# Performance work log

Measured on AMD Instinct MI355X. Metric: run time of the kernel, lower is better.

## Reference

```python
import jax, jax.numpy as jnp
import numpy as np

NUM_FREQS = 6

def posenc(x, num_freqs):
    freqs = (2.0 ** jnp.arange(num_freqs)).astype(x.dtype)  # [F]
    ang = x[..., None] * freqs                               # [N, D, F]
    enc = jnp.concatenate([jnp.sin(ang), jnp.cos(ang)], axis=-1)  # [N, D, 2F]
    return enc.reshape(x.shape[0], -1)

def setup_inputs() -> dict:
    key = jax.random.key(0)
    k1, k2, k3 = jax.random.split(key, 3)
    N, D, C = 200000, 6, 256
    E = D * 2 * NUM_FREQS  # 72
    X = jax.random.normal(k1, (N, D), dtype=jnp.float32)
    linear_mappings = jax.random.normal(k2, (3 * C, E), dtype=jnp.float32) * 0.05
    centroids = jax.random.normal(k3, (C, 3), dtype=jnp.float32)
    return {"X": X, "linear_mappings": linear_mappings, "centroids": centroids}

def reference(X, linear_mappings, centroids):
    N = X.shape[0]
    encoded_X = posenc(X, NUM_FREQS)                         # [N, E]
    rgb_clusters = encoded_X @ linear_mappings.T             # [N, 3C]
    rgb_clusters = rgb_clusters.reshape(N, -1, 3)            # [N, C, 3]
    # scores = centroids @ X[:, :3].T  -> softmax over clusters per point
    scores = X[:, :3] @ centroids.T                          # [N, C] (== scores.T in torch code)
    attention_weights = jax.nn.softmax(scores, axis=-1)      # [N, C]
    # torch does diagonal(attn @ rgb_clusters).T == per-row contraction:
    rgb = jnp.einsum('nc,ncd->nd', attention_weights, rgb_clusters)  # [N, 3]
    return rgb
```

## Files before the change

### kernel.cpp

```cpp
#include <hip/hip_runtime.h>
#include <math.h>


#define NCLUST   256
#define M_BLK    128
#define THREADS  256
#define NTILES   15
#define BG_BYTES (NTILES * 8 * 64 * 16)
#define ENC_STRIDE 168

typedef __attribute__((ext_vector_type(8))) short bfrag_t;
typedef __attribute__((ext_vector_type(4))) float cfrag_t;

static __device__ __forceinline__ unsigned int f2bf_u(float f) {
    unsigned int u = __float_as_uint(f);
    u += 0x7fffu + ((u >> 16) & 1u);
    return u >> 16;
}
static __device__ __forceinline__ unsigned int f2bf2(float lo, float hi) {
    return f2bf_u(lo) | (f2bf_u(hi) << 16);
}
static __device__ __forceinline__ float bf2f(unsigned short s) {
    return __uint_as_float(((unsigned int)s) << 16);
}
static __device__ __forceinline__ void glds16(const void* g, void* l) {
    __builtin_amdgcn_global_load_lds(
        (const __attribute__((address_space(1))) unsigned int*)g,
        (__attribute__((address_space(3))) unsigned int*)l, 16, 0, 0);
}

__global__ void prep_kernel(const float* __restrict__ W, uint4* __restrict__ Bg) {
    const int u = blockIdx.x * 256 + threadIdx.x;
    if (u >= NTILES * 8 * 64) return;
    const int lane = u & 63, ks = (u >> 6) & 7, tile = u >> 9;
    const int ln = lane & 15, q = lane >> 4;
    const int jp = tile * 16 + ln;
    const int d  = jp / 80;
    const int e  = jp - d * 80;
    const int c0 = ks * 32 + q * 8;
    unsigned int w[4] = {0u, 0u, 0u, 0u};
    if (e < 72) {
#pragma unroll
        for (int i = 0; i < 4; ++i) {
            float f0 = W[((c0 + 2 * i)     * 3 + d) * 72 + e];
            float f1 = W[((c0 + 2 * i + 1) * 3 + d) * 72 + e];
            w[i] = f2bf2(f0, f1);
        }
    }
    Bg[u] = make_uint4(w[0], w[1], w[2], w[3]);
}

__global__ __launch_bounds__(THREADS, 2) void rgb_attn_mfma(
    const float* __restrict__ X,
    const float* __restrict__ cent,
    const void* __restrict__ Bg,
    float* __restrict__ out, int N)
{
    __shared__ __align__(16) unsigned char encL[M_BLK * ENC_STRIDE];
    __shared__ __align__(16) unsigned char ABbuf[16384];
    __shared__ float denomL[M_BLK * 2];

    const int tid  = threadIdx.x;
    const int lane = tid & 63;
    const int wv   = tid >> 6;
    const int q    = lane >> 4;
    const int ln   = lane & 15;

    const int pt  = tid & 127;
    const int h   = tid >> 7;
    const int gpt = blockIdx.x * M_BLK + pt;
    const int gp  = (gpt < N) ? gpt : (N - 1);

    float x[6];
#pragma unroll
    for (int k = 0; k < 6; ++k) x[k] = X[gp * 6 + k];

    {
        const int row = tid >> 1, half = tid & 1;
        *(uint2*)(encL + row * ENC_STRIDE + 144 + half * 8) = make_uint2(0u, 0u);
    }
#pragma unroll
    for (int k = 0; k < 3; ++k) {
        const int dd = 3 * h + k;
        const float xv = x[dd];
        float s0,c0,s1,c1,s2,c2,s3,c3,s4,c4,s5,c5;
        __sincosf(xv *  1.0f, &s0, &c0);
        __sincosf(xv *  2.0f, &s1, &c1);
        __sincosf(xv *  4.0f, &s2, &c2);
        __sincosf(xv *  8.0f, &s3, &c3);
        __sincosf(xv * 16.0f, &s4, &c4);
        __sincosf(xv * 32.0f, &s5, &c5);
        unsigned char* rp = encL + pt * ENC_STRIDE + dd * 24;
        *(uint2*)(rp +  0) = make_uint2(f2bf2(s0, s1), f2bf2(s2, s3));
        *(uint2*)(rp +  8) = make_uint2(f2bf2(s4, s5), f2bf2(c0, c1));
        *(uint2*)(rp + 16) = make_uint2(f2bf2(c2, c3), f2bf2(c4, c5));
    }

    bfrag_t afrag[2][8];
    float dpart = 0.0f;
    uint4* AB4 = (uint4*)ABbuf;
#pragma unroll
    for (int p = 0; p < 4; ++p) {
        unsigned int pk[16];
#pragma unroll
        for (int i = 0; i < 16; ++i) {
            const int c0 = p * 64 + h * 32 + 2 * i;
            float sa = fmaf(x[0], cent[c0*3+0], fmaf(x[1], cent[c0*3+1], x[2]*cent[c0*3+2]));
            float sb = fmaf(x[0], cent[c0*3+3], fmaf(x[1], cent[c0*3+4], x[2]*cent[c0*3+5]));
            float ea = __expf(sa), eb_ = __expf(sb);
            dpart += ea + eb_;
            pk[i] = f2bf2(ea, eb_);
        }
        const int bu = ((pt >> 4) * 2 + h) * 64 + (pt & 15);
#pragma unroll
        for (int qq = 0; qq < 4; ++qq)
            AB4[bu + qq * 16] = make_uint4(pk[qq*4+0], pk[qq*4+1], pk[qq*4+2], pk[qq*4+3]);
        if (p == 3) denomL[pt * 2 + h] = dpart;
        __syncthreads();
#pragma unroll
        for (int mt = 0; mt < 2; ++mt)
#pragma unroll
            for (int kw = 0; kw < 2; ++kw)
                afrag[mt][2*p+kw] = *(const bfrag_t*)
                    (ABbuf + (((2*wv+mt)*2 + kw)*64 + lane)*16);
        __syncthreads();
    }

    float part[3][2][4] = {};

#define CONSUME_TILE(T, CT) { \
        cfrag_t a0 = {0.f,0.f,0.f,0.f}, a1 = {0.f,0.f,0.f,0.f}; \
        _Pragma("unroll") \
        for (int ks = 0; ks < 8; ++ks) { \
            const bfrag_t b = *(const bfrag_t*) \
                (ABbuf + (((CT)*8 + ks)*64 + lane)*16); \
            a0 = __builtin_amdgcn_mfma_f32_16x16x32_bf16(afrag[0][ks], b, a0, 0,0,0); \
            a1 = __builtin_amdgcn_mfma_f32_16x16x32_bf16(afrag[1][ks], b, a1, 0,0,0); \
        } \
        const int ebx = ((T) % 5) * 16 + ln; \
        _Pragma("unroll") \
        for (int mt = 0; mt < 2; ++mt) \
        _Pragma("unroll") \
        for (int r = 0; r < 4; ++r) { \
            const int pm = (2*wv + mt)*16 + q*4 + r; \
            const unsigned short us = *(const unsigned short*)(encL + pm*ENC_STRIDE + ebx*2); \
            part[(T)/5][mt][r] = fmaf((mt ? a1[r] : a0[r]), bf2f(us), part[(T)/5][mt][r]); \
        } \
    }

#define STAGE_CHUNK(CC, UNITS) { \
        __syncthreads(); \
        _Pragma("unroll") \
        for (int i = 0; i < 256; i += 64) { \
            if (i < (UNITS) / 4) { \
                const int u = wv * ((UNITS) / 4) + i + lane; \
                glds16((const char*)Bg + ((CC)*1024 + u)*16, (char*)ABbuf + u*16); \
            } } \
        __syncthreads(); \
    }

#define DO_CHUNK_FULL(CC) { \
        STAGE_CHUNK(CC, 1024); \
        CONSUME_TILE(2*(CC), 0); \
        CONSUME_TILE(2*(CC)+1, 1); \
    }

    DO_CHUNK_FULL(0) DO_CHUNK_FULL(1) DO_CHUNK_FULL(2) DO_CHUNK_FULL(3)
    DO_CHUNK_FULL(4) DO_CHUNK_FULL(5) DO_CHUNK_FULL(6)
    { STAGE_CHUNK(7, 512); CONSUME_TILE(14, 0); }

#pragma unroll
    for (int mask = 1; mask <= 8; mask <<= 1)
#pragma unroll
        for (int d = 0; d < 3; ++d)
#pragma unroll
            for (int mt = 0; mt < 2; ++mt)
#pragma unroll
                for (int r = 0; r < 4; ++r)
                    part[d][mt][r] += __shfl_xor(part[d][mt][r], mask, 64);

    if (ln == 0) {
#pragma unroll
        for (int mt = 0; mt < 2; ++mt)
#pragma unroll
            for (int r = 0; r < 4; ++r) {
                const int pm = (2*wv + mt)*16 + q*4 + r;
                const int g  = blockIdx.x * M_BLK + pm;
                if (g < N) {
                    const float inv = 1.0f / (denomL[pm*2] + denomL[pm*2+1]);
                    out[g*3+0] = part[0][mt][r] * inv;
                    out[g*3+1] = part[1][mt][r] * inv;
                    out[g*3+2] = part[2][mt][r] * inv;
                }
            }
    }
}

__global__ __launch_bounds__(256) void rgb_attn_fallback(
    const float* __restrict__ X, const float* __restrict__ W,
    const float* __restrict__ cent, float* __restrict__ out, int N)
{
    const int n = blockIdx.x * 256 + threadIdx.x;
    const bool valid = (n < N);
    float x[6];
#pragma unroll
    for (int k = 0; k < 6; ++k) x[k] = valid ? X[n * 6 + k] : 0.0f;
    float enc[72];
#pragma unroll
    for (int d = 0; d < 6; ++d)
#pragma unroll
        for (int f = 0; f < 6; ++f) {
            float s, c;
            __sincosf(x[d] * (float)(1 << f), &s, &c);
            enc[d*12+f] = s; enc[d*12+6+f] = c;
        }
    float acc0 = 0, acc1 = 0, acc2 = 0, denom = 0;
#pragma unroll 1
    for (int c = 0; c < NCLUST; ++c) {
        float s = fmaf(x[0], cent[c*3], fmaf(x[1], cent[c*3+1], x[2]*cent[c*3+2]));
        float ew = __expf(s);
        const float* w = W + c * 216;
        float d0 = 0, d1 = 0, d2 = 0;
#pragma unroll
        for (int e = 0; e < 72; ++e) {
            float ee = enc[e];
            d0 = fmaf(ee, w[e], d0);
            d1 = fmaf(ee, w[72 + e], d1);
            d2 = fmaf(ee, w[144 + e], d2);
        }
        denom += ew;
        acc0 = fmaf(ew, d0, acc0); acc1 = fmaf(ew, d1, acc1); acc2 = fmaf(ew, d2, acc2);
    }
    if (valid) {
        float inv = 1.0f / denom;
        out[n*3+0] = acc0*inv; out[n*3+1] = acc1*inv; out[n*3+2] = acc2*inv;
    }
}

extern "C" void kernel_launch(void* const* d_in, const int* in_sizes, int n_in,
                              void* d_out, int out_size, void* d_ws, size_t ws_size,
                              hipStream_t stream)
{
    const float* X    = (const float*)d_in[0];
    const float* W    = (const float*)d_in[1];
    const float* cent = (const float*)d_in[2];
    float* out = (float*)d_out;
    const int N = in_sizes[0] / 6;

    if (ws_size >= (size_t)BG_BYTES) {
        uint4* Bg = (uint4*)d_ws;
        prep_kernel<<<(NTILES * 8 * 64 + 255) / 256, 256, 0, stream>>>(W, Bg);
        const int blocks = (N + M_BLK - 1) / M_BLK;
        rgb_attn_mfma<<<blocks, THREADS, 0, stream>>>(X, cent, (const void*)Bg, out, N);
    } else {
        rgb_attn_fallback<<<(N + 255) / 256, 256, 0, stream>>>(X, W, cent, out, N);
    }
}
```

Baseline: 131.4 us.

## Build A fragments in registers and double-buffer B tiles per MFMA tile

Each lane now computes its softmax-numerator A fragments directly in registers from vectorized centroid loads, which removes the LDS round-trip and the four syncthreads of the old A staging. B tiles are streamed as 8KB tiles into a double buffer so the next tile's global-to-LDS load overlaps the current MFMAs, replacing the coarse 16KB stage-and-wait chunks. The encoding is stored transposed so it can be read with vector loads, and it uses double-angle recurrences instead of six sincos calls. Denominators are reduced with shuffles rather than through LDS. The recurrence can accumulate error at the high frequencies, and there is still one barrier per tile.

New measurement: 116.6 us. 1.13x faster.

```diff
diff --git a/kernel.cpp b/kernel.cpp
--- a/kernel.cpp
+++ b/kernel.cpp
@@ -7,18 +7,17 @@
 #define THREADS  256
 #define NTILES   15
 #define BG_BYTES (NTILES * 8 * 64 * 16)
-#define ENC_STRIDE 168
+#define ET_STRIDE 264
 
 typedef __attribute__((ext_vector_type(8))) short bfrag_t;
 typedef __attribute__((ext_vector_type(4))) float cfrag_t;
-
-static __device__ __forceinline__ unsigned int f2bf_u(float f) {
-    unsigned int u = __float_as_uint(f);
-    u += 0x7fffu + ((u >> 16) & 1u);
-    return u >> 16;
+typedef __attribute__((ext_vector_type(4))) unsigned int uifrag_t;
+
+static __device__ __forceinline__ unsigned short f2bf1(float f) {
+    return __builtin_bit_cast(unsigned short, (__bf16)f);
 }
 static __device__ __forceinline__ unsigned int f2bf2(float lo, float hi) {
-    return f2bf_u(lo) | (f2bf_u(hi) << 16);
+    return (unsigned int)f2bf1(lo) | ((unsigned int)f2bf1(hi) << 16);
 }
 static __device__ __forceinline__ float bf2f(unsigned short s) {
     return __uint_as_float(((unsigned int)s) << 16);
@@ -56,9 +55,8 @@
     const void* __restrict__ Bg,
     float* __restrict__ out, int N)
 {
-    __shared__ __align__(16) unsigned char encL[M_BLK * ENC_STRIDE];
-    __shared__ __align__(16) unsigned char ABbuf[16384];
-    __shared__ float denomL[M_BLK * 2];
+    __shared__ __align__(16) unsigned char encT[80 * ET_STRIDE];
+    __shared__ __align__(16) unsigned char Bbuf[2][8192];
 
     const int tid  = threadIdx.x;
     const int lane = tid & 63;
@@ -66,108 +64,116 @@
     const int q    = lane >> 4;
     const int ln   = lane & 15;
 
-    const int pt  = tid & 127;
-    const int h   = tid >> 7;
-    const int gpt = blockIdx.x * M_BLK + pt;
-    const int gp  = (gpt < N) ? gpt : (N - 1);
-
-    float x[6];
-#pragma unroll
-    for (int k = 0; k < 6; ++k) x[k] = X[gp * 6 + k];
+#pragma unroll
+    for (int i = 0; i < 2; ++i) {
+        const int u = i * 256 + wv * 64 + lane;
+        glds16((const char*)Bg + u * 16, (char*)Bbuf[0] + u * 16);
+    }
 
     {
-        const int row = tid >> 1, half = tid & 1;
-        *(uint2*)(encL + row * ENC_STRIDE + 144 + half * 8) = make_uint2(0u, 0u);
-    }
-#pragma unroll
-    for (int k = 0; k < 3; ++k) {
-        const int dd = 3 * h + k;
-        const float xv = x[dd];
-        float s0,c0,s1,c1,s2,c2,s3,c3,s4,c4,s5,c5;
-        __sincosf(xv *  1.0f, &s0, &c0);
-        __sincosf(xv *  2.0f, &s1, &c1);
-        __sincosf(xv *  4.0f, &s2, &c2);
-        __sincosf(xv *  8.0f, &s3, &c3);
-        __sincosf(xv * 16.0f, &s4, &c4);
-        __sincosf(xv * 32.0f, &s5, &c5);
-        unsigned char* rp = encL + pt * ENC_STRIDE + dd * 24;
-        *(uint2*)(rp +  0) = make_uint2(f2bf2(s0, s1), f2bf2(s2, s3));
-        *(uint2*)(rp +  8) = make_uint2(f2bf2(s4, s5), f2bf2(c0, c1));
-        *(uint2*)(rp + 16) = make_uint2(f2bf2(c2, c3), f2bf2(c4, c5));
-    }
-
-    bfrag_t afrag[2][8];
-    float dpart = 0.0f;
-    uint4* AB4 = (uint4*)ABbuf;
-#pragma unroll
-    for (int p = 0; p < 4; ++p) {
-        unsigned int pk[16];
-#pragma unroll
-        for (int i = 0; i < 16; ++i) {
-            const int c0 = p * 64 + h * 32 + 2 * i;
-            float sa = fmaf(x[0], cent[c0*3+0], fmaf(x[1], cent[c0*3+1], x[2]*cent[c0*3+2]));
-            float sb = fmaf(x[0], cent[c0*3+3], fmaf(x[1], cent[c0*3+4], x[2]*cent[c0*3+5]));
-            float ea = __expf(sa), eb_ = __expf(sb);
-            dpart += ea + eb_;
-            pk[i] = f2bf2(ea, eb_);
-        }
-        const int bu = ((pt >> 4) * 2 + h) * 64 + (pt & 15);
-#pragma unroll
-        for (int qq = 0; qq < 4; ++qq)
-            AB4[bu + qq * 16] = make_uint4(pk[qq*4+0], pk[qq*4+1], pk[qq*4+2], pk[qq*4+3]);
-        if (p == 3) denomL[pt * 2 + h] = dpart;
-        __syncthreads();
-#pragma unroll
-        for (int mt = 0; mt < 2; ++mt)
-#pragma unroll
-            for (int kw = 0; kw < 2; ++kw)
-                afrag[mt][2*p+kw] = *(const bfrag_t*)
-                    (ABbuf + (((2*wv+mt)*2 + kw)*64 + lane)*16);
-        __syncthreads();
-    }
+        const int pt  = tid & 127;
+        const int h   = tid >> 7;
+        const int gpt = blockIdx.x * M_BLK + pt;
+        const int gp  = (gpt < N) ? gpt : (N - 1);
+        unsigned char* colp = encT + pt * 2;
+#pragma unroll
+        for (int k = 0; k < 3; ++k) {
+            const int dd = 3 * h + k;
+            const float xv = X[gp * 6 + dd];
+            float s[6], c[6];
+            __sincosf(xv, &s[0], &c[0]);
+#pragma unroll
+            for (int f = 1; f < 6; ++f) {
+                s[f] = 2.0f * s[f-1] * c[f-1];
+                c[f] = 1.0f - 2.0f * s[f-1] * s[f-1];
+            }
+#pragma unroll
+            for (int f = 0; f < 6; ++f) {
+                *(unsigned short*)(colp + (dd*12 + f)     * ET_STRIDE) = f2bf1(s[f]);
+                *(unsigned short*)(colp + (dd*12 + 6 + f) * ET_STRIDE) = f2bf1(c[f]);
+            }
+        }
+        *(uint2*)(encT + (72 + (tid >> 5)) * ET_STRIDE + (tid & 31) * 8) = make_uint2(0u, 0u);
+    }
+
+    uifrag_t afrag[2][8];
+    float dA = 0.0f, dB = 0.0f;
+    {
+        const int pm0 = (2 * wv) * 16 + ln;
+        const int g0a = blockIdx.x * M_BLK + pm0;
+        const int g0  = (g0a < N) ? g0a : (N - 1);
+        const int g1a = g0a + 16;
+        const int g1  = (g1a < N) ? g1a : (N - 1);
+        const float2 xy0 = *(const float2*)(X + g0 * 6);
+        const float  z0  = X[g0 * 6 + 2];
+        const float2 xy1 = *(const float2*)(X + g1 * 6);
+        const float  z1  = X[g1 * 6 + 2];
+        const float4* c4base = (const float4*)cent;
+#pragma unroll
+        for (int g = 0; g < 8; ++g) {
+            const float4* c4 = c4base + (6 * q + 24 * g);
+            const float4 v0 = c4[0], v1 = c4[1], v2 = c4[2];
+            const float4 v3 = c4[3], v4 = c4[4], v5 = c4[5];
+            float cx[8], cy[8], cz[8];
+            cx[0]=v0.x; cy[0]=v0.y; cz[0]=v0.z;
+            cx[1]=v0.w; cy[1]=v1.x; cz[1]=v1.y;
+            cx[2]=v1.z; cy[2]=v1.w; cz[2]=v2.x;
+            cx[3]=v2.y; cy[3]=v2.z; cz[3]=v2.w;
+            cx[4]=v3.x; cy[4]=v3.y; cz[4]=v3.z;
+            cx[5]=v3.w; cy[5]=v4.x; cz[5]=v4.y;
+            cx[6]=v4.z; cy[6]=v4.w; cz[6]=v5.x;
+            cx[7]=v5.y; cy[7]=v5.z; cz[7]=v5.w;
+            float ea[8], eb[8];
+#pragma unroll
+            for (int j = 0; j < 8; ++j) {
+                ea[j] = __expf(fmaf(xy0.x, cx[j], fmaf(xy0.y, cy[j], z0 * cz[j])));
+                eb[j] = __expf(fmaf(xy1.x, cx[j], fmaf(xy1.y, cy[j], z1 * cz[j])));
+                dA += ea[j]; dB += eb[j];
+            }
+#pragma unroll
+            for (int w = 0; w < 4; ++w) {
+                afrag[0][g][w] = f2bf2(ea[2*w], ea[2*w+1]);
+                afrag[1][g][w] = f2bf2(eb[2*w], eb[2*w+1]);
+            }
+        }
+    }
+
+    __syncthreads();
 
     float part[3][2][4] = {};
-
-#define CONSUME_TILE(T, CT) { \
-        cfrag_t a0 = {0.f,0.f,0.f,0.f}, a1 = {0.f,0.f,0.f,0.f}; \
-        _Pragma("unroll") \
-        for (int ks = 0; ks < 8; ++ks) { \
-            const bfrag_t b = *(const bfrag_t*) \
-                (ABbuf + (((CT)*8 + ks)*64 + lane)*16); \
-            a0 = __builtin_amdgcn_mfma_f32_16x16x32_bf16(afrag[0][ks], b, a0, 0,0,0); \
-            a1 = __builtin_amdgcn_mfma_f32_16x16x32_bf16(afrag[1][ks], b, a1, 0,0,0); \
-        } \
-        const int ebx = ((T) % 5) * 16 + ln; \
-        _Pragma("unroll") \
-        for (int mt = 0; mt < 2; ++mt) \
-        _Pragma("unroll") \
-        for (int r = 0; r < 4; ++r) { \
-            const int pm = (2*wv + mt)*16 + q*4 + r; \
-            const unsigned short us = *(const unsigned short*)(encL + pm*ENC_STRIDE + ebx*2); \
-            part[(T)/5][mt][r] = fmaf((mt ? a1[r] : a0[r]), bf2f(us), part[(T)/5][mt][r]); \
-        } \
-    }
-
-#define STAGE_CHUNK(CC, UNITS) { \
-        __syncthreads(); \
-        _Pragma("unroll") \
-        for (int i = 0; i < 256; i += 64) { \
-            if (i < (UNITS) / 4) { \
-                const int u = wv * ((UNITS) / 4) + i + lane; \
-                glds16((const char*)Bg + ((CC)*1024 + u)*16, (char*)ABbuf + u*16); \
-            } } \
-        __syncthreads(); \
-    }
-
-#define DO_CHUNK_FULL(CC) { \
-        STAGE_CHUNK(CC, 1024); \
-        CONSUME_TILE(2*(CC), 0); \
-        CONSUME_TILE(2*(CC)+1, 1); \
-    }
-
-    DO_CHUNK_FULL(0) DO_CHUNK_FULL(1) DO_CHUNK_FULL(2) DO_CHUNK_FULL(3)
-    DO_CHUNK_FULL(4) DO_CHUNK_FULL(5) DO_CHUNK_FULL(6)
-    { STAGE_CHUNK(7, 512); CONSUME_TILE(14, 0); }
+#pragma unroll
+    for (int t = 0; t < NTILES; ++t) {
+        if (t) __syncthreads();
+        if (t < NTILES - 1) {
+#pragma unroll
+            for (int i = 0; i < 2; ++i) {
+                const int u = i * 256 + wv * 64 + lane;
+                glds16((const char*)Bg + ((t + 1) * 512 + u) * 16,
+                       (char*)Bbuf[(t + 1) & 1] + u * 16);
+            }
+        }
+        cfrag_t a0 = {0.f,0.f,0.f,0.f}, a1 = {0.f,0.f,0.f,0.f};
+#pragma unroll
+        for (int ks = 0; ks < 8; ++ks) {
+            const bfrag_t b = *(const bfrag_t*)(Bbuf[t & 1] + (ks * 64 + lane) * 16);
+            a0 = __builtin_amdgcn_mfma_f32_16x16x32_bf16(
+                     __builtin_bit_cast(bfrag_t, afrag[0][ks]), b, a0, 0, 0, 0);
+            a1 = __builtin_amdgcn_mfma_f32_16x16x32_bf16(
+                     __builtin_bit_cast(bfrag_t, afrag[1][ks]), b, a1, 0, 0, 0);
+        }
+        const int d  = t / 5;
+        const int er = (t % 5) * 16 + ln;
+#pragma unroll
+        for (int mt = 0; mt < 2; ++mt) {
+            const ushort4 ev = *(const ushort4*)(encT + er * ET_STRIDE
+                                   + ((2 * wv + mt) * 16 + q * 4) * 2);
+            const cfrag_t a = mt ? a1 : a0;
+            part[d][mt][0] = fmaf(a[0], bf2f(ev.x), part[d][mt][0]);
+            part[d][mt][1] = fmaf(a[1], bf2f(ev.y), part[d][mt][1]);
+            part[d][mt][2] = fmaf(a[2], bf2f(ev.z), part[d][mt][2]);
+            part[d][mt][3] = fmaf(a[3], bf2f(ev.w), part[d][mt][3]);
+        }
+    }
 
 #pragma unroll
     for (int mask = 1; mask <= 8; mask <<= 1)
@@ -179,18 +185,28 @@
                 for (int r = 0; r < 4; ++r)
                     part[d][mt][r] += __shfl_xor(part[d][mt][r], mask, 64);
 
+    dA += __shfl_xor(dA, 16, 64); dA += __shfl_xor(dA, 32, 64);
+    dB += __shfl_xor(dB, 16, 64); dB += __shfl_xor(dB, 32, 64);
+    const float iA = 1.0f / dA;
+    const float iB = 1.0f / dB;
+    float invr[2][4];
+#pragma unroll
+    for (int r = 0; r < 4; ++r) {
+        invr[0][r] = __shfl(iA, q * 4 + r, 64);
+        invr[1][r] = __shfl(iB, q * 4 + r, 64);
+    }
+
     if (ln == 0) {
 #pragma unroll
         for (int mt = 0; mt < 2; ++mt)
 #pragma unroll
             for (int r = 0; r < 4; ++r) {
-                const int pm = (2*wv + mt)*16 + q*4 + r;
+                const int pm = (2 * wv + mt) * 16 + q * 4 + r;
                 const int g  = blockIdx.x * M_BLK + pm;
                 if (g < N) {
-                    const float inv = 1.0f / (denomL[pm*2] + denomL[pm*2+1]);
-                    out[g*3+0] = part[0][mt][r] * inv;
-                    out[g*3+1] = part[1][mt][r] * inv;
-                    out[g*3+2] = part[2][mt][r] * inv;
+                    out[g*3+0] = part[0][mt][r] * invr[mt][r];
+                    out[g*3+1] = part[1][mt][r] * invr[mt][r];
+                    out[g*3+2] = part[2][mt][r] * invr[mt][r];
                 }
             }
     }
```
